# Kernel tuning notes

Hardware: AMD Instinct MI355X
Metric: run time of the kernel (lower is better)

The kernel has to match this reference:

```python
import jax, jax.numpy as jnp
import numpy as np

# Dimensions: B tokens, D=d_model, H=4*D expert hidden, E experts, K=top_k
B, D, H, E, K = 2048, 1024, 4096, 8, 2


def setup_inputs() -> dict:
    key = jax.random.key(0)
    ks = jax.random.split(key, 5)
    scale = 0.02
    return {
        "moe_inp": jax.random.normal(ks[0], (B, D), jnp.float32),
        # NaiveGate: single Linear(d_model -> num_expert)
        "gate_w": jax.random.normal(ks[1], (E, D), jnp.float32) * scale,
        "gate_b": jnp.zeros((E,), jnp.float32),
        # Fused experts: per-expert htoh4 (D->H) and h4toh (H->D).
        # Stored pre-transposed relative to torch Linear.weight for x @ W.
        "w1": jax.random.normal(ks[2], (E, D, H), jnp.float32) * scale,
        "b1": jnp.zeros((E, H), jnp.float32),
        "w2": jax.random.normal(ks[3], (E, H, D), jnp.float32) * scale,
        "b2": jnp.zeros((E, D), jnp.float32),
    }


def reference(moe_inp, gate_w, gate_b, w1, b1, w2, b2):
    # --- NaiveGate: linear -> top-k -> softmax over selected logits ---
    logits = moe_inp @ gate_w.T + gate_b            # [B, E]
    top_val, top_idx = jax.lax.top_k(logits, K)     # [B, K]
    gate_score = jax.nn.softmax(top_val, axis=-1)   # [B, K]

    # --- Grouped expert FFN (all experts on all tokens; combine weights
    #     are zero for non-selected experts so the math matches exact
    #     token dispatch + per-expert GEMM + weighted bmm combine) ---
    h = jnp.einsum('bd,edh->ebh', moe_inp, w1) + b1[:, None, :]   # [E, B, H]
    h = jax.nn.gelu(h, approximate=False)
    y = jnp.einsum('ebh,ehd->ebd', h, w2) + b2[:, None, :]        # [E, B, D]

    # combine weight per (token, expert): sum of gate scores of matching top-k slots
    combine = jnp.sum(jax.nn.one_hot(top_idx, E, dtype=moe_inp.dtype)
                      * gate_score[..., None], axis=1)            # [B, E]
    out = jnp.einsum('be,ebd->bd', combine, y)                    # [B, D]
    return out
```

## Files before the change

### kernel.cpp

```cpp
#include <hip/hip_runtime.h>
#include <math.h>

#define B_TOK 2048
#define DMODEL 1024
#define HDIM 4096
#define NEXP 8
#define TOPK 2

#define BM 128
#define BK 64
#define MAX_TILES 40

typedef __attribute__((ext_vector_type(8))) short bf16x8;
typedef __attribute__((ext_vector_type(4))) float f32x4;

__device__ __forceinline__ unsigned short f2b(float f) {
  unsigned u = __builtin_bit_cast(unsigned, f);
  unsigned r = (u + 0x7FFFu + ((u >> 16) & 1u)) >> 16;
  return (unsigned short)r;
}

__device__ __forceinline__ void load_lds16(const void* g, void* l) {
  __builtin_amdgcn_global_load_lds(
      (const __attribute__((address_space(1))) unsigned int*)g,
      (__attribute__((address_space(3))) unsigned int*)l, 16, 0, 0);
}

__device__ __forceinline__ float gelu_fast(float v) {
  float x = v * 0.70710678118654752f;
  float ax = fabsf(x);
  float t = 1.0f / (1.0f + 0.3275911f * ax);
  float e = exp2f(-ax * ax * 1.4426950408889634f);
  float p = t * (0.254829592f +
                 t * (-0.284496736f +
                      t * (1.421413741f +
                           t * (-1.453152027f + t * 1.061405429f))));
  float er = 1.0f - p * e;
  er = copysignf(er, x);
  return 0.5f * v * (1.0f + er);
}

__global__ __launch_bounds__(256) void gate_kernel(
    const float* __restrict__ x, const float* __restrict__ gw,
    const float* __restrict__ gb, int* __restrict__ idx2,
    float* __restrict__ sc2, float* __restrict__ out) {
  int lane = threadIdx.x & 63;
  int w = threadIdx.x >> 6;
  int b = blockIdx.x * 4 + w;
  {
    float4 z = make_float4(0.f, 0.f, 0.f, 0.f);
    float* orow = out + (size_t)(blockIdx.x * 4) * DMODEL;
#pragma unroll
    for (int i = 0; i < 4; ++i)
      *(float4*)(orow + i * 1024 + threadIdx.x * 4) = z;
  }
  double acc[NEXP];
#pragma unroll
  for (int e = 0; e < NEXP; ++e) acc[e] = 0.0;
  const float* xr = x + (size_t)b * DMODEL;
#pragma unroll
  for (int i = 0; i < 4; ++i) {
    float4 xv = *(const float4*)(xr + i * 256 + lane * 4);
#pragma unroll
    for (int e = 0; e < NEXP; ++e) {
      float4 wv = *(const float4*)(gw + e * DMODEL + i * 256 + lane * 4);
      acc[e] += (double)xv.x * wv.x + (double)xv.y * wv.y +
                (double)xv.z * wv.z + (double)xv.w * wv.w;
    }
  }
#pragma unroll
  for (int e = 0; e < NEXP; ++e) {
    double v = acc[e];
    for (int o = 1; o < 64; o <<= 1) v += __shfl_xor(v, o, 64);
    acc[e] = v + (double)gb[e];
  }
  if (lane == 0) {
    int i0 = 0;
    double v0 = acc[0];
#pragma unroll
    for (int e = 1; e < NEXP; ++e)
      if (acc[e] > v0) { v0 = acc[e]; i0 = e; }
    int i1 = -1;
    double v1 = -1e300;
#pragma unroll
    for (int e = 0; e < NEXP; ++e)
      if (e != i0 && acc[e] > v1) { v1 = acc[e]; i1 = e; }
    double t = exp(v1 - v0);
    float s0 = (float)(1.0 / (1.0 + t));
    float s1 = (float)(t / (1.0 + t));
    idx2[b * 2] = i0;
    idx2[b * 2 + 1] = i1;
    sc2[b * 2] = s0;
    sc2[b * 2 + 1] = s1;
  }
}

__global__ __launch_bounds__(256) void route_kernel(
    const int* __restrict__ idx2, const float* __restrict__ sc2,
    int* __restrict__ tile_map, int* __restrict__ ntiles,
    int* __restrict__ pos_of, int* __restrict__ row_of,
    float* __restrict__ s_of) {
  __shared__ int lc[NEXP][257];
  __shared__ int offs[NEXP + 1];
  const int tid = threadIdx.x;
  const int base = tid * 16;
#pragma unroll
  for (int e = 0; e < NEXP; ++e) lc[e][tid + 1] = 0;
  if (tid < NEXP) lc[tid][0] = 0;
  __syncthreads();
  int loc[16];
#pragma unroll
  for (int j = 0; j < 16; ++j) {
    int e = idx2[base + j];
    loc[j] = e;
    atomicAdd(&lc[e][tid + 1], 1);
  }
  __syncthreads();
  if (tid < NEXP) {
    int s = 0;
    for (int i = 1; i <= 256; ++i) {
      s += lc[tid][i];
      lc[tid][i] = s;
    }
  }
  __syncthreads();
  if (tid == 0) {
    offs[0] = 0;
    for (int e = 0; e < NEXP; ++e) offs[e + 1] = offs[e] + lc[e][256];
    int tt = 0;
    for (int e = 0; e < NEXP; ++e) {
      int cnt = lc[e][256];
      int bse = offs[e];
      for (int t = 0; t * BM < cnt; ++t) {
        tile_map[tt * 4 + 0] = e;
        tile_map[tt * 4 + 1] = bse + t * BM;
        tile_map[tt * 4 + 2] = (cnt - t * BM) < BM ? (cnt - t * BM) : BM;
        tile_map[tt * 4 + 3] = 0;
        ++tt;
      }
    }
    *ntiles = tt;
  }
  __syncthreads();
#pragma unroll
  for (int e = 0; e < NEXP; ++e) lc[e][tid] += offs[e];
  __syncthreads();
#pragma unroll
  for (int j = 0; j < 16; ++j) {
    int e = loc[j];
    int p = lc[e][tid];
    lc[e][tid] = p + 1;
    int t = base + j;
    pos_of[t] = p;
    row_of[p] = t >> 1;
    s_of[p] = sc2[t];
  }
}

__global__ __launch_bounds__(256) void gather_kernel(
    const float* __restrict__ x, const int* __restrict__ row_of,
    unsigned short* __restrict__ Xp) {
  int r = blockIdx.x;
  int tok = row_of[r];
  int c = threadIdx.x * 4;
  float4 v = *(const float4*)(x + (size_t)tok * DMODEL + c);
  ushort4 o = make_ushort4(f2b(v.x), f2b(v.y), f2b(v.z), f2b(v.w));
  *(ushort4*)(Xp + (size_t)r * DMODEL + c) = o;
}

__global__ __launch_bounds__(256) void convT_kernel(
    const float* __restrict__ W, unsigned short* __restrict__ Wt, int Kd, int Nd,
    int tilesN, int cpx) {
  __shared__ unsigned L[64 * 33];
  int bidx = (blockIdx.x & 7) * cpx + (blockIdx.x >> 3);
  int nt = bidx % tilesN;
  int r2 = bidx / tilesN;
  int tilesK = Kd >> 6;
  int kt = r2 % tilesK;
  int e = r2 / tilesK;
  int tid = threadIdx.x;

  const float* src = W + (long)e * Kd * Nd + (long)(kt * 64) * Nd + nt * 64;
  int kp = tid >> 3;
  int nb = tid & 7;
  const float* r0 = src + (long)(2 * kp) * Nd + nb * 8;
  const float* r1 = r0 + Nd;
  float4 va0 = *(const float4*)r0;
  float4 va1 = *(const float4*)(r0 + 4);
  float4 vb0 = *(const float4*)r1;
  float4 vb1 = *(const float4*)(r1 + 4);
  const float* a = (const float*)&va0;
  const float* bq = (const float*)&vb0;
#pragma unroll
  for (int j = 0; j < 4; ++j) {
    unsigned p = (unsigned)f2b(a[j]) | ((unsigned)f2b(bq[j]) << 16);
    L[(nb * 8 + j) * 33 + kp] = p;
  }
  const float* a2 = (const float*)&va1;
  const float* b2 = (const float*)&vb1;
#pragma unroll
  for (int j = 0; j < 4; ++j) {
    unsigned p = (unsigned)f2b(a2[j]) | ((unsigned)f2b(b2[j]) << 16);
    L[(nb * 8 + 4 + j) * 33 + kp] = p;
  }
  __syncthreads();
  int n = tid >> 2;
  int part = tid & 3;
  unsigned q[8];
#pragma unroll
  for (int j = 0; j < 8; ++j) q[j] = L[n * 33 + part * 8 + j];
  unsigned* dst = (unsigned*)(Wt + (long)e * Nd * Kd + (long)(nt * 64 + n) * Kd +
                              kt * 64) +
                  part * 8;
  *(uint4*)dst = make_uint4(q[0], q[1], q[2], q[3]);
  *(uint4*)(dst + 4) = make_uint4(q[4], q[5], q[6], q[7]);
}

template <int BN_, int WM, int WN, bool GELU, int OMODE>
__global__ __launch_bounds__(256) void gemm_bt(
    const unsigned short* __restrict__ A, int lda,
    const unsigned short* __restrict__ Bt, long strideB,
    const float* __restrict__ bias, int strideBias, void* __restrict__ Cout,
    int ldc, const int* __restrict__ row_of, const float* __restrict__ s_of,
    const int* __restrict__ tile_map, const int* __restrict__ ntiles, int N,
    int K) {
  const int nb = N / BN_;
  const int tile = blockIdx.x / nb;
  if (tile >= *ntiles) return;
  const int ct = blockIdx.x % nb;
  const int e = tile_map[tile * 4 + 0];
  const int row0 = tile_map[tile * 4 + 1];
  const int rows = tile_map[tile * 4 + 2];
  const int n0 = ct * BN_;
  const unsigned short* B_e = Bt + (long)e * strideB + (long)n0 * K;

  __shared__ __align__(16) unsigned short Asm[BM * BK];
  __shared__ __align__(16) unsigned short Bsm[BN_ * BK];

  const int tid = threadIdx.x;
  const int lane = tid & 63;
  const int w = tid >> 6;
  const int WTM = BM / WM, WTN = BN_ / WN;
  const int wr = (w / WN) * WTM;
  const int wc = (w % WN) * WTN;
  const int MR = WTM / 16, NR = WTN / 16;
  const int l15 = lane & 15;
  const int l4 = lane >> 4;

  f32x4 acc[MR][NR] = {};

  for (int k0 = 0; k0 < K; k0 += BK) {
#pragma unroll
    for (int it = 0; it < 4; ++it) {
      int c = it * 256 + tid;
      int r = c >> 3, kc = c & 7;
      int kcs = kc ^ (r & 7);
      load_lds16(A + (size_t)(row0 + r) * lda + k0 + kcs * 8,
                 ((char*)Asm) + (size_t)(it * 256 + w * 64) * 16);
    }
#pragma unroll
    for (int it = 0; it < BN_ / 32; ++it) {
      int c = it * 256 + tid;
      int r = c >> 3, kc = c & 7;
      int kcs = kc ^ (r & 7);
      load_lds16(B_e + (size_t)r * K + k0 + kcs * 8,
                 ((char*)Bsm) + (size_t)(it * 256 + w * 64) * 16);
    }
    __syncthreads();
#pragma unroll
    for (int kk = 0; kk < 2; ++kk) {
      bf16x8 a[MR], b[NR];
#pragma unroll
      for (int m = 0; m < MR; ++m) {
        int row = wr + m * 16 + l15;
        int ch = (kk * 4 + l4) ^ (l15 & 7);
        a[m] = *(const bf16x8*)&Asm[row * BK + ch * 8];
      }
#pragma unroll
      for (int n = 0; n < NR; ++n) {
        int row = wc + n * 16 + l15;
        int ch = (kk * 4 + l4) ^ (l15 & 7);
        b[n] = *(const bf16x8*)&Bsm[row * BK + ch * 8];
      }
#pragma unroll
      for (int m = 0; m < MR; ++m)
#pragma unroll
        for (int n = 0; n < NR; ++n)
          acc[m][n] =
              __builtin_amdgcn_mfma_f32_16x16x32_bf16(a[m], b[n], acc[m][n], 0, 0, 0);
    }
    __syncthreads();
  }

  const float* bias_e = bias + (long)e * strideBias;
#pragma unroll
  for (int m = 0; m < MR; ++m) {
#pragma unroll
    for (int i = 0; i < 4; ++i) {
      int r = wr + m * 16 + l4 * 4 + i;
      if (r < rows) {
        if (OMODE == 2) {
          int tok = row_of[row0 + r];
          float s = s_of[row0 + r];
          float* op = (float*)Cout + (size_t)tok * ldc;
#pragma unroll
          for (int n = 0; n < NR; ++n) {
            int cg = n0 + wc + n * 16 + l15;
            float v = acc[m][n][i] + bias_e[cg];
            atomicAdd(&op[cg], s * v);
          }
        } else {
          size_t grow = (size_t)(row0 + r) * ldc;
#pragma unroll
          for (int n = 0; n < NR; ++n) {
            int cg = n0 + wc + n * 16 + l15;
            float v = acc[m][n][i] + bias_e[cg];
            if (GELU) v = gelu_fast(v);
            if (OMODE == 1)
              ((unsigned short*)Cout)[grow + cg] = f2b(v);
            else
              ((float*)Cout)[grow + cg] = v;
          }
        }
      }
    }
  }
}

extern "C" void kernel_launch(void* const* d_in, const int* in_sizes, int n_in,
                              void* d_out, int out_size, void* d_ws, size_t ws_size,
                              hipStream_t stream) {
  const float* x = (const float*)d_in[0];
  const float* gw = (const float*)d_in[1];
  const float* gb = (const float*)d_in[2];
  const float* w1 = (const float*)d_in[3];
  const float* b1 = (const float*)d_in[4];
  const float* w2 = (const float*)d_in[5];
  const float* b2 = (const float*)d_in[6];
  float* out = (float*)d_out;
  char* ws = (char*)d_ws;

  int* ntiles = (int*)(ws + 128);
  int* tile_map = (int*)(ws + 256);
  int* idx2 = (int*)(ws + 4096);
  float* sc2 = (float*)(ws + 20480);
  int* pos_of = (int*)(ws + 36864);
  int* row_of = (int*)(ws + 53248);
  float* s_of = (float*)(ws + 73728);
  unsigned short* Xp = (unsigned short*)(ws + 131072);
  unsigned short* H1 = (unsigned short*)(ws + 8781824);
  unsigned short* Wt = (unsigned short*)(ws + 43384832);
  if (ws_size < 110493696ULL) return;

  gate_kernel<<<B_TOK / 4, 256, 0, stream>>>(x, gw, gb, idx2, sc2, out);
  route_kernel<<<1, 256, 0, stream>>>(idx2, sc2, tile_map, ntiles, pos_of,
                                      row_of, s_of);
  gather_kernel<<<B_TOK * TOPK, 256, 0, stream>>>(x, row_of, Xp);

  convT_kernel<<<NEXP * (DMODEL / 64) * (HDIM / 64), 256, 0, stream>>>(
      w1, Wt, DMODEL, HDIM, HDIM / 64, NEXP * (DMODEL / 64) * (HDIM / 64) / 8);
  gemm_bt<128, 2, 2, true, 1><<<MAX_TILES * (HDIM / 128), 256, 0, stream>>>(
      Xp, DMODEL, Wt, (long)HDIM * DMODEL, b1, HDIM, H1, HDIM, nullptr, nullptr,
      tile_map, ntiles, HDIM, DMODEL);
  convT_kernel<<<NEXP * (HDIM / 64) * (DMODEL / 64), 256, 0, stream>>>(
      w2, Wt, HDIM, DMODEL, DMODEL / 64, NEXP * (HDIM / 64) * (DMODEL / 64) / 8);
  gemm_bt<64, 4, 1, false, 2><<<MAX_TILES * (DMODEL / 64), 256, 0, stream>>>(
      H1, HDIM, Wt, (long)DMODEL * HDIM, b2, DMODEL, out, DMODEL, row_of, s_of,
      tile_map, ntiles, DMODEL, HDIM);
}
```

Before: 275.9 us.

## Add 256-row tile GEMM1 kernel with 512 threads and separate tile map

Adds a second routing tile map with 256-row tiles and a new first-layer GEMM kernel that uses 512 threads, 8 waves each computing a 64x64 output block, over a 256x128 block tile. Larger M tiles halve how often each weight tile is reloaded per expert and increase MFMA work per barrier. The cost is fewer blocks, so the grid may not fill all CUs, and more padding waste for experts whose token counts are not multiples of 256. Rows past the tile's count may read beyond the expert's segment, but those results are masked at store.

```diff
diff --git a/kernel.cpp b/kernel.cpp
--- a/kernel.cpp
+++ b/kernel.cpp
@@ -10,6 +10,7 @@
 #define BM 128
 #define BK 64
 #define MAX_TILES 40
+#define MAX_T256 24
 
 typedef __attribute__((ext_vector_type(8))) short bf16x8;
 typedef __attribute__((ext_vector_type(4))) float f32x4;
@@ -98,6 +99,7 @@
 __global__ __launch_bounds__(256) void route_kernel(
     const int* __restrict__ idx2, const float* __restrict__ sc2,
     int* __restrict__ tile_map, int* __restrict__ ntiles,
+    int* __restrict__ tm256, int* __restrict__ nt256,
     int* __restrict__ pos_of, int* __restrict__ row_of,
     float* __restrict__ s_of) {
   __shared__ int lc[NEXP][257];
@@ -127,7 +129,7 @@
   if (tid == 0) {
     offs[0] = 0;
     for (int e = 0; e < NEXP; ++e) offs[e + 1] = offs[e] + lc[e][256];
-    int tt = 0;
+    int tt = 0, t2 = 0;
     for (int e = 0; e < NEXP; ++e) {
       int cnt = lc[e][256];
       int bse = offs[e];
@@ -138,8 +140,16 @@
         tile_map[tt * 4 + 3] = 0;
         ++tt;
       }
+      for (int t = 0; t * 256 < cnt; ++t) {
+        tm256[t2 * 4 + 0] = e;
+        tm256[t2 * 4 + 1] = bse + t * 256;
+        tm256[t2 * 4 + 2] = (cnt - t * 256) < 256 ? (cnt - t * 256) : 256;
+        tm256[t2 * 4 + 3] = 0;
+        ++t2;
+      }
     }
     *ntiles = tt;
+    *nt256 = t2;
   }
   __syncthreads();
 #pragma unroll
@@ -214,6 +224,98 @@
                   part * 8;
   *(uint4*)dst = make_uint4(q[0], q[1], q[2], q[3]);
   *(uint4*)(dst + 4) = make_uint4(q[4], q[5], q[6], q[7]);
+}
+
+__global__ __launch_bounds__(512) void gemm1_wide(
+    const unsigned short* __restrict__ A, int lda,
+    const unsigned short* __restrict__ Bt, long strideB,
+    const float* __restrict__ bias, unsigned short* __restrict__ Cout, int ldc,
+    const int* __restrict__ tm256, const int* __restrict__ nt256, int N,
+    int K) {
+  const int nb = N / 128;
+  const int tile = blockIdx.x / nb;
+  if (tile >= *nt256) return;
+  const int ct = blockIdx.x % nb;
+  const int e = tm256[tile * 4 + 0];
+  const int row0 = tm256[tile * 4 + 1];
+  const int rows = tm256[tile * 4 + 2];
+  const int n0 = ct * 128;
+  const unsigned short* B_e = Bt + (long)e * strideB + (long)n0 * K;
+
+  __shared__ __align__(16) unsigned short Asm[256 * BK];
+  __shared__ __align__(16) unsigned short Bsm[128 * BK];
+
+  const int tid = threadIdx.x;
+  const int lane = tid & 63;
+  const int w = tid >> 6;
+  const int wr = (w >> 1) * 64;
+  const int wc = (w & 1) * 64;
+  const int l15 = lane & 15;
+  const int l4 = lane >> 4;
+
+  f32x4 acc[4][4] = {};
+
+  for (int k0 = 0; k0 < K; k0 += BK) {
+#pragma unroll
+    for (int it = 0; it < 4; ++it) {
+      int c = it * 512 + tid;
+      int r = c >> 3, kc = c & 7;
+      int kcs = kc ^ (r & 7);
+      load_lds16(A + (size_t)(row0 + r) * lda + k0 + kcs * 8,
+                 ((char*)Asm) + (size_t)(it * 512 + w * 64) * 16);
+    }
+#pragma unroll
+    for (int it = 0; it < 2; ++it) {
+      int c = it * 512 + tid;
+      int r = c >> 3, kc = c & 7;
+      int kcs = kc ^ (r & 7);
+      load_lds16(B_e + (size_t)r * K + k0 + kcs * 8,
+                 ((char*)Bsm) + (size_t)(it * 512 + w * 64) * 16);
+    }
+    __syncthreads();
+#pragma unroll
+    for (int kk = 0; kk < 2; ++kk) {
+      bf16x8 a[4], b[4];
+#pragma unroll
+      for (int m = 0; m < 4; ++m) {
+        int row = wr + m * 16 + l15;
+        int ch = (kk * 4 + l4) ^ (l15 & 7);
+        a[m] = *(const bf16x8*)&Asm[row * BK + ch * 8];
+      }
+#pragma unroll
+      for (int n = 0; n < 4; ++n) {
+        int row = wc + n * 16 + l15;
+        int ch = (kk * 4 + l4) ^ (l15 & 7);
+        b[n] = *(const bf16x8*)&Bsm[row * BK + ch * 8];
+      }
+#pragma unroll
+      for (int m = 0; m < 4; ++m)
+#pragma unroll
+        for (int n = 0; n < 4; ++n)
+          acc[m][n] =
+              __builtin_amdgcn_mfma_f32_16x16x32_bf16(a[m], b[n], acc[m][n], 0, 0, 0);
+    }
+    __syncthreads();
+  }
+
+  const float* bias_e = bias + (long)e * HDIM;
+#pragma unroll
+  for (int m = 0; m < 4; ++m) {
+#pragma unroll
+    for (int i = 0; i < 4; ++i) {
+      int r = wr + m * 16 + l4 * 4 + i;
+      if (r < rows) {
+        size_t grow = (size_t)(row0 + r) * ldc;
+#pragma unroll
+        for (int n = 0; n < 4; ++n) {
+          int cg = n0 + wc + n * 16 + l15;
+          float v = acc[m][n][i] + bias_e[cg];
+          v = gelu_fast(v);
+          Cout[grow + cg] = f2b(v);
+        }
+      }
+    }
+  }
 }
 
 template <int BN_, int WM, int WN, bool GELU, int OMODE>
@@ -341,7 +443,9 @@
   char* ws = (char*)d_ws;
 
   int* ntiles = (int*)(ws + 128);
+  int* nt256 = (int*)(ws + 132);
   int* tile_map = (int*)(ws + 256);
+  int* tm256 = (int*)(ws + 2048);
   int* idx2 = (int*)(ws + 4096);
   float* sc2 = (float*)(ws + 20480);
   int* pos_of = (int*)(ws + 36864);
@@ -352,16 +456,18 @@
   unsigned short* Wt = (unsigned short*)(ws + 43384832);
   if (ws_size < 110493696ULL) return;
 
+  (void)&gemm_bt<128, 2, 2, true, 1>;
+
   gate_kernel<<<B_TOK / 4, 256, 0, stream>>>(x, gw, gb, idx2, sc2, out);
-  route_kernel<<<1, 256, 0, stream>>>(idx2, sc2, tile_map, ntiles, pos_of,
-                                      row_of, s_of);
+  route_kernel<<<1, 256, 0, stream>>>(idx2, sc2, tile_map, ntiles, tm256, nt256,
+                                      pos_of, row_of, s_of);
   gather_kernel<<<B_TOK * TOPK, 256, 0, stream>>>(x, row_of, Xp);
 
   convT_kernel<<<NEXP * (DMODEL / 64) * (HDIM / 64), 256, 0, stream>>>(
       w1, Wt, DMODEL, HDIM, HDIM / 64, NEXP * (DMODEL / 64) * (HDIM / 64) / 8);
-  gemm_bt<128, 2, 2, true, 1><<<MAX_TILES * (HDIM / 128), 256, 0, stream>>>(
-      Xp, DMODEL, Wt, (long)HDIM * DMODEL, b1, HDIM, H1, HDIM, nullptr, nullptr,
-      tile_map, ntiles, HDIM, DMODEL);
+  gemm1_wide<<<MAX_T256 * (HDIM / 128), 512, 0, stream>>>(
+      Xp, DMODEL, Wt, (long)HDIM * DMODEL, b1, H1, HDIM, tm256, nt256, HDIM,
+      DMODEL);
   convT_kernel<<<NEXP * (HDIM / 64) * (DMODEL / 64), 256, 0, stream>>>(
       w2, Wt, HDIM, DMODEL, DMODEL / 64, NEXP * (HDIM / 64) * (DMODEL / 64) / 8);
   gemm_bt<64, 4, 1, false, 2><<<MAX_TILES * (DMODEL / 64), 256, 0, stream>>>(
```

After: 270.3 us. -2.0%, faster.
